# Kernel optimization log

Hardware: AMD Instinct MI355X
Metric: run time of the kernel (lower is better)

Reference implementation:

```python
import jax, jax.numpy as jnp
import numpy as np

B, S, D = 2, 2048, 2048
QC, KVC = 16, 4          # query heads, kv heads (GQA)
HD = D // QC             # head_dim = 128
FF = 8192                # ff_dim = 4 * model_dim
EPS = 1e-5


def rotate_every_two(x):
    x1 = x[..., ::2]
    x2 = x[..., 1::2]
    return jnp.stack((-x2, x1), axis=-1).reshape(*x.shape[:-1], -1)


def apply_rope(x, seq_len, sin, cos):
    sin = sin[:seq_len]
    cos = cos[:seq_len]
    return x * cos + rotate_every_two(x) * sin


def rmsnorm(x, w, eps=EPS):
    xf = x.astype(jnp.float32)
    xf = xf * jax.lax.rsqrt(jnp.square(xf).mean(-1, keepdims=True) + eps)
    return xf.astype(x.dtype) * w


def attention(x, mask, sin, cos, wqkv, wo):
    b, s, d = x.shape
    kv_repeat = QC // KVC
    qkv = x @ wqkv
    q = qkv[..., :D].reshape(b, s, kv_repeat, KVC, HD)
    q = jnp.moveaxis(q, 1, 3)                       # (b, rep, kvc, s, hd)
    q = apply_rope(q, s, sin, cos)
    k, v = jnp.split(qkv[..., D:], 2, axis=-1)
    k = k.reshape(b, s, KVC, HD).swapaxes(1, 2)     # (b, kvc, s, hd)
    v = v.reshape(b, s, KVC, HD).swapaxes(1, 2)
    k = apply_rope(k, s, sin, cos) * (HD ** -0.5)
    k = k[:, None]                                  # (b, 1, kvc, s, hd)
    v = v[:, None]
    a = q @ k.swapaxes(-2, -1)                      # (b, rep, kvc, s, s)
    a = a + mask[:s, :s]
    a = jax.nn.softmax(a, axis=-1)
    o = a @ v                                       # (b, rep, kvc, s, hd)
    o = o.reshape(b, QC, s, HD).swapaxes(1, 2).reshape(b, s, d)
    return o @ wo


def ffn(x, wk, wv):
    k = jnp.square(jax.nn.relu(x @ wk))
    return k @ wv


def setup_inputs() -> dict:
    key = jax.random.key(0)
    ks = jax.random.split(key, 6)
    std = 0.02
    x = jax.random.normal(ks[0], (B, S, D), jnp.float32)
    wqkv = std * jax.random.normal(ks[1], (D, D + 2 * KVC * HD), jnp.float32)
    wo = std * jax.random.normal(ks[2], (D, D), jnp.float32)
    ffn_wk = std * jax.random.normal(ks[3], (D, FF), jnp.float32)
    ffn_wv = std * jax.random.normal(ks[4], (FF, D), jnp.float32)
    norm1_w = jnp.ones((D,), jnp.float32)
    norm2_w = jnp.ones((D,), jnp.float32)
    # GPT-J style interleaved RoPE tables of shape (S, HD)
    pos = jnp.arange(S, dtype=jnp.float32)
    inv_freq = 1.0 / (10000.0 ** (jnp.arange(0, HD, 2, dtype=jnp.float32) / HD))
    freqs = pos[:, None] * inv_freq[None, :]
    rope_sin = jnp.repeat(jnp.sin(freqs), 2, axis=-1)
    rope_cos = jnp.repeat(jnp.cos(freqs), 2, axis=-1)
    # additive causal mask
    mask = jnp.where(jnp.tril(jnp.ones((S, S), bool)), 0.0, -1e9).astype(jnp.float32)
    return dict(x=x, mask=mask, rope_sin=rope_sin, rope_cos=rope_cos,
                wqkv=wqkv, wo=wo, norm1_w=norm1_w, norm2_w=norm2_w,
                ffn_wk=ffn_wk, ffn_wv=ffn_wv)


def reference(x, mask, rope_sin, rope_cos, wqkv, wo, norm1_w, norm2_w, ffn_wk, ffn_wv):
    # pre-norm residual block
    x = x + attention(rmsnorm(x, norm1_w), mask, rope_sin, rope_cos, wqkv, wo)
    x = x + ffn(rmsnorm(x, norm2_w), ffn_wk, ffn_wv)
    return x
```

## Files before the change

### kernel.cpp

```cpp
#include <hip/hip_runtime.h>
#include <hip/hip_bf16.h>
#include <cstdint>
#include <cstddef>
#include <type_traits>

typedef __hip_bfloat16 bf16;
typedef float f32x4 __attribute__((ext_vector_type(4)));
typedef short s16x8 __attribute__((ext_vector_type(8)));

#define BB 2
#define SS 2048
#define DD 2048
#define QCH 16
#define KVH 4
#define HD 128
#define FF 8192

__device__ __forceinline__ float b2f(bf16 v) { return __bfloat162float(v); }
__device__ __forceinline__ bf16 f2b(float v) { return __float2bfloat16(v); }

__device__ __forceinline__ void gl_lds16(const void* g, void* l) {
    __builtin_amdgcn_global_load_lds((const __attribute__((address_space(1))) void*)g,
                                     (__attribute__((address_space(3))) void*)l,
                                     16, 0, 0);
}

#define GBAR __builtin_amdgcn_s_barrier()
#define LGK0 do { asm volatile("s_waitcnt lgkmcnt(0)" ::: "memory"); __builtin_amdgcn_sched_barrier(0); } while (0)
#define VM8  asm volatile("s_waitcnt vmcnt(8)" ::: "memory")

__global__ __launch_bounds__(256) void transpose_cast(const float* __restrict__ src,
                                                      bf16* __restrict__ dst,
                                                      int K, int N) {
    __shared__ float t[32][33];
    int n0 = blockIdx.x * 32, k0 = blockIdx.y * 32;
    int tx = threadIdx.x, ty = threadIdx.y;
#pragma unroll
    for (int j = 0; j < 4; ++j)
        t[ty + j * 8][tx] = src[(size_t)(k0 + ty + j * 8) * N + n0 + tx];
    __syncthreads();
#pragma unroll
    for (int j = 0; j < 4; ++j)
        dst[(size_t)(n0 + ty + j * 8) * K + k0 + tx] = f2b(t[tx][ty + j * 8]);
}

__global__ __launch_bounds__(256) void rmsnorm_k(const float* __restrict__ x,
                                                 const float* __restrict__ w,
                                                 bf16* __restrict__ out) {
    int row = blockIdx.x;
    int tid = threadIdx.x;
    const float* xr = x + (size_t)row * DD + tid * 8;
    f32x4 a0 = *(const f32x4*)xr;
    f32x4 a1 = *(const f32x4*)(xr + 4);
    float f[8];
    float ss = 0.f;
#pragma unroll
    for (int i = 0; i < 4; ++i) { f[i] = a0[i]; f[i + 4] = a1[i]; }
#pragma unroll
    for (int i = 0; i < 8; ++i) ss += f[i] * f[i];
#pragma unroll
    for (int off = 32; off > 0; off >>= 1) ss += __shfl_down(ss, off);
    __shared__ float red[4];
    int lane = tid & 63, wv_ = tid >> 6;
    if (lane == 0) red[wv_] = ss;
    __syncthreads();
    float tot = red[0] + red[1] + red[2] + red[3];
    float scale = rsqrtf(tot * (1.0f / DD) + 1e-5f);
#pragma unroll
    for (int i = 0; i < 8; ++i) {
        int col = tid * 8 + i;
        out[(size_t)row * DD + col] = f2b(f[i] * scale * w[col]);
    }
}

__global__ __launch_bounds__(256) void rmsnorm_add3(const float* __restrict__ pa,
                                                    const float* __restrict__ pb,
                                                    const float* __restrict__ xr,
                                                    const float* __restrict__ w,
                                                    float* __restrict__ x1,
                                                    bf16* __restrict__ out) {
    int row = blockIdx.x;
    int tid = threadIdx.x;
    size_t base = (size_t)row * DD + tid * 8;
    f32x4 a0 = *(const f32x4*)(pa + base);
    f32x4 a1 = *(const f32x4*)(pa + base + 4);
    f32x4 b0 = *(const f32x4*)(pb + base);
    f32x4 b1 = *(const f32x4*)(pb + base + 4);
    f32x4 c0 = *(const f32x4*)(xr + base);
    f32x4 c1 = *(const f32x4*)(xr + base + 4);
    a0 = a0 + b0 + c0;
    a1 = a1 + b1 + c1;
    *(f32x4*)(x1 + base) = a0;
    *(f32x4*)(x1 + base + 4) = a1;
    float f[8];
    float ss = 0.f;
#pragma unroll
    for (int i = 0; i < 4; ++i) { f[i] = a0[i]; f[i + 4] = a1[i]; }
#pragma unroll
    for (int i = 0; i < 8; ++i) ss += f[i] * f[i];
#pragma unroll
    for (int off = 32; off > 0; off >>= 1) ss += __shfl_down(ss, off);
    __shared__ float red[4];
    int lane = tid & 63, wv_ = tid >> 6;
    if (lane == 0) red[wv_] = ss;
    __syncthreads();
    float tot = red[0] + red[1] + red[2] + red[3];
    float scale = rsqrtf(tot * (1.0f / DD) + 1e-5f);
#pragma unroll
    for (int i = 0; i < 8; ++i) {
        int col = tid * 8 + i;
        out[base + i] = f2b(f[i] * scale * w[col]);
    }
}

__global__ __launch_bounds__(256) void add3_k(const float* __restrict__ pa,
                                              const float* __restrict__ pb,
                                              const float* __restrict__ x1,
                                              float* __restrict__ o, int n4) {
    int stride = gridDim.x * 256;
    for (int i = blockIdx.x * 256 + threadIdx.x; i < n4; i += stride) {
        f32x4 a = ((const f32x4*)pa)[i];
        f32x4 b = ((const f32x4*)pb)[i];
        f32x4 c = ((const f32x4*)x1)[i];
        ((f32x4*)o)[i] = a + b + c;
    }
}

__global__ __launch_bounds__(256) void rope_scatter(const bf16* __restrict__ qkv,
                                                    const float* __restrict__ rsin,
                                                    const float* __restrict__ rcos,
                                                    bf16* __restrict__ q_r,
                                                    bf16* __restrict__ k_r,
                                                    bf16* __restrict__ v_t) {
    int p = blockIdx.x * 256 + threadIdx.x;
    int row = p / 1536;
    int c2 = p - row * 1536;
    int col = c2 * 2;
    int b = row >> 11, s = row & 2047;
    size_t qbase = (size_t)row * 3072 + col;
    float e = b2f(qkv[qbase]);
    float o = b2f(qkv[qbase + 1]);
    if (col < 2048) {
        int h = col >> 7, hd = col & 127;
        float cs = rcos[s * HD + hd];
        float sn = rsin[s * HD + hd];
        size_t base = (((size_t)(b * QCH + h)) * SS + s) * HD + hd;
        q_r[base]     = f2b(e * cs - o * sn);
        q_r[base + 1] = f2b(o * cs + e * sn);
    } else if (col < 2560) {
        int cc = col - 2048;
        int kc = cc >> 7, hd = cc & 127;
        float cs = rcos[s * HD + hd];
        float sn = rsin[s * HD + hd];
        const float kscale = 0.08838834764831845f;
        size_t base = (((size_t)(b * KVH + kc)) * SS + s) * HD + hd;
        k_r[base]     = f2b((e * cs - o * sn) * kscale);
        k_r[base + 1] = f2b((o * cs + e * sn) * kscale);
    } else {
        int cc = col - 2560;
        int kc = cc >> 7, hd = cc & 127;
        size_t base = (((size_t)(b * KVH + kc)) * HD + hd) * SS + s;
        v_t[base]      = qkv[qbase];
        v_t[base + SS] = qkv[qbase + 1];
    }
}

template <int EPI, typename CT>
__global__ __launch_bounds__(512) void gemm256(const bf16* __restrict__ A,
                                               const bf16* __restrict__ Bt,
                                               CT* __restrict__ C,
                                               CT* __restrict__ Cp,
                                               int M, int N, int KH, int ldk,
                                               int nsplit) {
    __shared__ __align__(16) bf16 As[2][2][8192];
    __shared__ __align__(16) bf16 Bs[2][2][8192];

    const int tid = threadIdx.x;
    const int w = tid >> 6, lane = tid & 63;
    const int lm = lane & 15, quad = lane >> 4;
    const int wm = w >> 2, wn = w & 3;

    const int cpx = gridDim.x >> 3;
    int sb = (blockIdx.x & 7) * cpx + (blockIdx.x >> 3);
    const int nbx = N >> 8;
    const int ntiles = (M >> 8) * nbx;
    const int kh = (nsplit == 2 && sb >= ntiles) ? 1 : 0;
    sb -= kh * ntiles;
    const int bx = sb % nbx, by = sb / nbx;
    const int m0 = by * 256, n0 = bx * 256;
    CT* Cw = kh ? Cp : C;

    const size_t LD2 = (size_t)ldk * 2;
    const int srow = tid >> 3;
    const int sboff = ((tid & 7) ^ (srow & 7)) * 16;
    const int NT = KH >> 6;

    const char* Abase = (const char*)A + (size_t)m0 * LD2 + (size_t)kh * KH * 2 + sboff;
    const char* Bbase = (const char*)Bt + (size_t)n0 * LD2 + (size_t)kh * KH * 2 + sboff;
    char* lAs = (char*)&As[0][0][0];
    char* lBs = (char*)&Bs[0][0][0];

    auto stA = [&](int db, int h, int t) {
#pragma unroll
        for (int j = 0; j < 2; ++j) {
            int row = h * 128 + j * 64 + srow;
            gl_lds16(Abase + (size_t)row * LD2 + (size_t)t * 128,
                     lAs + (db * 2 + h) * 16384 + j * 8192 + tid * 16);
        }
    };
    auto stB = [&](int db, int h, int t) {
#pragma unroll
        for (int j = 0; j < 2; ++j) {
            int row = h * 128 + j * 64 + srow;
            gl_lds16(Bbase + (size_t)row * LD2 + (size_t)t * 128,
                     lBs + (db * 2 + h) * 16384 + j * 8192 + tid * 16);
        }
    };

    const int c0 = (quad ^ (lm & 7)) * 16;
    const int c1 = ((4 + quad) ^ (lm & 7)) * 16;

    s16x8 a0[4][2], a1[4][2], b0[2][2], b1[2][2];
    f32x4 acc[8][4];
    const f32x4 zero = {0.f, 0.f, 0.f, 0.f};
#pragma unroll
    for (int i = 0; i < 8; ++i)
#pragma unroll
        for (int j = 0; j < 4; ++j) acc[i][j] = zero;

    auto ldA = [&](s16x8 (&a)[4][2], int db, int mh) {
        const char* base = lAs + (db * 2 + wm) * 16384 + (mh * 64 + lm) * 128;
#pragma unroll
        for (int mi = 0; mi < 4; ++mi) {
            a[mi][0] = *(const s16x8*)(base + mi * 2048 + c0);
            a[mi][1] = *(const s16x8*)(base + mi * 2048 + c1);
        }
    };
    auto ldB = [&](s16x8 (&b)[2][2], int db, int nh) {
        const char* base = lBs + (db * 2 + (wn >> 1)) * 16384 + ((wn & 1) * 64 + nh * 32 + lm) * 128;
#pragma unroll
        for (int ni = 0; ni < 2; ++ni) {
            b[ni][0] = *(const s16x8*)(base + ni * 2048 + c0);
            b[ni][1] = *(const s16x8*)(base + ni * 2048 + c1);
        }
    };
    auto mm = [&](s16x8 (&a)[4][2], s16x8 (&b)[2][2], int mh, int nh) {
#pragma unroll
        for (int mi = 0; mi < 4; ++mi)
#pragma unroll
            for (int ni = 0; ni < 2; ++ni)
#pragma unroll
                for (int kk = 0; kk < 2; ++kk)
                    acc[mh * 4 + mi][nh * 2 + ni] = __builtin_amdgcn_mfma_f32_16x16x32_bf16(
                        a[mi][kk], b[ni][kk], acc[mh * 4 + mi][nh * 2 + ni], 0, 0, 0);
    };

    stA(0, 0, 0); stA(0, 1, 0); stB(0, 0, 0); stB(0, 1, 0);
    stA(1, 0, 1); stA(1, 1, 1); stB(1, 0, 1); stB(1, 1, 1);
    VM8;
    GBAR;

    const int NI = NT >> 1;
#pragma unroll 1
    for (int i = 0; i < NI; ++i) {
        int tA = 2 * i + 2; if (tA >= NT) tA = 0;
        int tB = 2 * i + 3; if (tB >= NT) tB = 0;
        ldA(a0, 0, 0); ldB(b0, 0, 0);
        GBAR; LGK0;
        __builtin_amdgcn_s_setprio(1); mm(a0, b0, 0, 0); __builtin_amdgcn_s_setprio(0);
        GBAR;
        ldA(a1, 0, 1); ldB(b1, 0, 1);
        GBAR; LGK0;
        __builtin_amdgcn_s_setprio(1); mm(a1, b1, 1, 1); __builtin_amdgcn_s_setprio(0);
        GBAR;
        stA(0, 0, tA); stA(0, 1, tA);
        GBAR;
        __builtin_amdgcn_s_setprio(1); mm(a0, b1, 0, 1); __builtin_amdgcn_s_setprio(0);
        GBAR;
        stB(0, 0, tA); stB(0, 1, tA);
        GBAR;
        __builtin_amdgcn_s_setprio(1); mm(a1, b0, 1, 0); __builtin_amdgcn_s_setprio(0);
        VM8;
        GBAR;
        ldA(a0, 1, 0); ldB(b0, 1, 0);
        GBAR; LGK0;
        __builtin_amdgcn_s_setprio(1); mm(a0, b0, 0, 0); __builtin_amdgcn_s_setprio(0);
        GBAR;
        ldA(a1, 1, 1); ldB(b1, 1, 1);
        GBAR; LGK0;
        __builtin_amdgcn_s_setprio(1); mm(a1, b1, 1, 1); __builtin_amdgcn_s_setprio(0);
        GBAR;
        stA(1, 0, tB); stA(1, 1, tB);
        GBAR;
        __builtin_amdgcn_s_setprio(1); mm(a0, b1, 0, 1); __builtin_amdgcn_s_setprio(0);
        GBAR;
        stB(1, 0, tB); stB(1, 1, tB);
        GBAR;
        __builtin_amdgcn_s_setprio(1); mm(a1, b0, 1, 0); __builtin_amdgcn_s_setprio(0);
        VM8;
        GBAR;
    }

#pragma unroll
    for (int mi = 0; mi < 8; ++mi)
#pragma unroll
        for (int ni = 0; ni < 4; ++ni) {
            int gr = m0 + wm * 128 + mi * 16 + quad * 4;
            int gc = n0 + wn * 64 + ni * 16 + lm;
#pragma unroll
            for (int r = 0; r < 4; ++r) {
                size_t idx = (size_t)(gr + r) * N + gc;
                float v = acc[mi][ni][r];
                if (EPI == 2) { v = fmaxf(v, 0.f); v = v * v; }
                if constexpr (std::is_same<CT, float>::value) Cw[idx] = v;
                else Cw[idx] = f2b(v);
            }
        }
}

__global__ __launch_bounds__(256) void attn_k(const bf16* __restrict__ q_r,
                                              const bf16* __restrict__ k_r,
                                              const bf16* __restrict__ v_t,
                                              bf16* __restrict__ o_buf) {
    __shared__ __align__(16) bf16 Ks[64 * 128];
    __shared__ __align__(16) bf16 Vs[128 * 64];
    __shared__ __align__(16) bf16 Ps[4][32 * 72];
    const int i = blockIdx.x;
    const int qt = i >> 5, hb = i & 31;
    const int h = hb & 15, b = hb >> 4;
    const int tid = threadIdx.x, w = tid >> 6, lane = tid & 63;
    const int lm = lane & 15, quad = lane >> 4;
    const int kvh = h & (KVH - 1);
    const int qw0 = qt * 128 + w * 32;
    bf16* Pw = &Ps[w][0];

    s16x8 aq[2][4];
#pragma unroll
    for (int mt = 0; mt < 2; ++mt) {
        const bf16* qp = q_r + (((size_t)(b * QCH + h)) * SS + qw0 + mt * 16 + lm) * HD + quad * 8;
#pragma unroll
        for (int c = 0; c < 4; ++c) aq[mt][c] = *(const s16x8*)(qp + c * 32);
    }

    const char* kbase = (const char*)(k_r + ((size_t)(b * KVH + kvh)) * SS * HD);
    const char* vbase = (const char*)(v_t + ((size_t)(b * KVH + kvh)) * HD * SS);

    const int krow = tid >> 4, kslot = tid & 15;
    const int ksrc_off = ((kslot ^ (krow & 15)) * 16);
    const int vrow = tid >> 3, vslot = tid & 7;

    const f32x4 zero = {0.f, 0.f, 0.f, 0.f};
    f32x4 accO[2][8];
#pragma unroll
    for (int mt = 0; mt < 2; ++mt)
#pragma unroll
        for (int ni = 0; ni < 8; ++ni) accO[mt][ni] = zero;
    float lp[2][4] = {{0.f, 0.f, 0.f, 0.f}, {0.f, 0.f, 0.f, 0.f}};

    const int ntiles = 2 * qt + 2;
    for (int kt = 0; kt < ntiles; ++kt) {
        const int kb = kt * 64;
#pragma unroll
        for (int j = 0; j < 4; ++j) {
            int kr = krow + j * 16;
            gl_lds16(kbase + (size_t)(kb + kr) * 256 + ksrc_off, (char*)Ks + tid * 16 + j * 4096);
        }
#pragma unroll
        for (int j = 0; j < 4; ++j) {
            int vr = vrow + j * 32;
            gl_lds16(vbase + (size_t)vr * (SS * 2) + kb * 2 + ((vslot ^ (vr & 7)) * 16),
                     (char*)Vs + tid * 16 + j * 4096);
        }
        __syncthreads();

        const bool active = (kb <= qw0 + 31);
        if (active) {
#pragma unroll
            for (int nt = 0; nt < 4; ++nt) {
                const int krl = nt * 16 + lm;
                s16x8 kf[4];
#pragma unroll
                for (int c = 0; c < 4; ++c)
                    kf[c] = *(const s16x8*)((char*)Ks + krl * 256 + (((c * 4 + quad) ^ lm) * 16));
                const int colk = kb + krl;
#pragma unroll
                for (int mt = 0; mt < 2; ++mt) {
                    f32x4 sc = zero;
#pragma unroll
                    for (int c = 0; c < 4; ++c)
                        sc = __builtin_amdgcn_mfma_f32_16x16x32_bf16(aq[mt][c], kf[c], sc, 0, 0, 0);
#pragma unroll
                    for (int r = 0; r < 4; ++r) {
                        int rowq = qw0 + mt * 16 + quad * 4 + r;
                        float p = (colk <= rowq) ? __expf(sc[r]) : 0.f;
                        lp[mt][r] += p;
                        Pw[(mt * 16 + quad * 4 + r) * 72 + nt * 16 + lm] = f2b(p);
                    }
                }
            }
            s16x8 pf[2][2];
#pragma unroll
            for (int mt = 0; mt < 2; ++mt)
#pragma unroll
                for (int kf2 = 0; kf2 < 2; ++kf2)
                    pf[mt][kf2] = *(const s16x8*)&Pw[(mt * 16 + lm) * 72 + kf2 * 32 + quad * 8];
#pragma unroll
            for (int ni = 0; ni < 8; ++ni) {
                const int vrl = ni * 16 + lm;
#pragma unroll
                for (int kf2 = 0; kf2 < 2; ++kf2) {
                    s16x8 vf = *(const s16x8*)((char*)Vs + vrl * 128 + (((kf2 * 4 + quad) ^ (lm & 7)) * 16));
#pragma unroll
                    for (int mt = 0; mt < 2; ++mt)
                        accO[mt][ni] = __builtin_amdgcn_mfma_f32_16x16x32_bf16(pf[mt][kf2], vf, accO[mt][ni], 0, 0, 0);
                }
            }
        }
        __syncthreads();
    }

#pragma unroll
    for (int mt = 0; mt < 2; ++mt)
#pragma unroll
        for (int r = 0; r < 4; ++r) {
            float l = lp[mt][r];
#pragma unroll
            for (int off = 1; off < 16; off <<= 1) l += __shfl_xor(l, off);
            lp[mt][r] = 1.f / l;
        }

#pragma unroll
    for (int mt = 0; mt < 2; ++mt)
#pragma unroll
        for (int ni = 0; ni < 8; ++ni)
#pragma unroll
            for (int r = 0; r < 4; ++r) {
                int s = qw0 + mt * 16 + quad * 4 + r;
                size_t idx = ((size_t)(b * SS + s)) * DD + h * HD + ni * 16 + lm;
                o_buf[idx] = f2b(accO[mt][ni][r] * lp[mt][r]);
            }
}

extern "C" void kernel_launch(void* const* d_in, const int* in_sizes, int n_in,
                              void* d_out, int out_size, void* d_ws, size_t ws_size,
                              hipStream_t stream) {
    const float* x    = (const float*)d_in[0];
    const float* rsin = (const float*)d_in[2];
    const float* rcos = (const float*)d_in[3];
    const float* wqkv = (const float*)d_in[4];
    const float* wo   = (const float*)d_in[5];
    const float* n1w  = (const float*)d_in[6];
    const float* n2w  = (const float*)d_in[7];
    const float* wk   = (const float*)d_in[8];
    const float* wv   = (const float*)d_in[9];
    float* out = (float*)d_out;

    char* ws = (char*)d_ws;
    size_t off = 0;
    auto allocb = [&](size_t elems) { bf16* p = (bf16*)(ws + off); off += elems * 2; return p; };
    auto allocf = [&](size_t elems) { float* p = (float*)(ws + off); off += elems * 4; return p; };
    bf16* wqkvT = allocb((size_t)3072 * 2048);
    bf16* woT   = allocb((size_t)2048 * 2048);
    bf16* wkT   = allocb((size_t)8192 * 2048);
    bf16* wvT   = allocb((size_t)2048 * 8192);
    bf16* xn    = allocb((size_t)4096 * 2048);
    bf16* qkv   = allocb((size_t)4096 * 3072);
    bf16* q_r   = allocb((size_t)BB * QCH * SS * HD);
    bf16* k_r   = allocb((size_t)BB * KVH * SS * HD);
    bf16* v_t   = allocb((size_t)BB * KVH * HD * SS);
    bf16* ffnh  = allocb((size_t)4096 * 8192);
    float* x1   = allocf((size_t)4096 * 2048);
    float* pwo = (float*)ffnh;
    float* pdn = (float*)qkv;

    dim3 tb(32, 8);
    transpose_cast<<<dim3(3072 / 32, 2048 / 32), tb, 0, stream>>>(wqkv, wqkvT, 2048, 3072);
    transpose_cast<<<dim3(2048 / 32, 2048 / 32), tb, 0, stream>>>(wo, woT, 2048, 2048);
    transpose_cast<<<dim3(8192 / 32, 2048 / 32), tb, 0, stream>>>(wk, wkT, 2048, 8192);
    transpose_cast<<<dim3(2048 / 32, 8192 / 32), tb, 0, stream>>>(wv, wvT, 8192, 2048);

    rmsnorm_k<<<4096, 256, 0, stream>>>(x, n1w, xn);
    gemm256<0, bf16><<<192, 512, 0, stream>>>(xn, wqkvT, qkv, qkv, 4096, 3072, 2048, 2048, 1);
    rope_scatter<<<(4096 * 1536) / 256, 256, 0, stream>>>(qkv, rsin, rcos, q_r, k_r, v_t);
    attn_k<<<512, 256, 0, stream>>>(q_r, k_r, v_t, qkv );
    gemm256<0, float><<<256, 512, 0, stream>>>(qkv, woT, x1, pwo, 4096, 2048, 1024, 2048, 2);
    rmsnorm_add3<<<4096, 256, 0, stream>>>(x1, pwo, x, n2w, x1, xn);
    gemm256<2, bf16><<<512, 512, 0, stream>>>(xn, wkT, ffnh, ffnh, 4096, 8192, 2048, 2048, 1);
    gemm256<0, float><<<256, 512, 0, stream>>>(ffnh, wvT, out, pdn, 4096, 2048, 4096, 8192, 2);
    add3_k<<<2048, 256, 0, stream>>>(out, pdn, x1, out, (4096 * 2048) / 4);
}
```

Before: 811.8 us.

## Restructure GEMM main loop into finer-grained staggered LDS/global prefetch schedule

```diff
diff --git a/kernel.cpp b/kernel.cpp
--- a/kernel.cpp
+++ b/kernel.cpp
@@ -27,7 +27,10 @@
 
 #define GBAR __builtin_amdgcn_s_barrier()
 #define LGK0 do { asm volatile("s_waitcnt lgkmcnt(0)" ::: "memory"); __builtin_amdgcn_sched_barrier(0); } while (0)
-#define VM8  asm volatile("s_waitcnt vmcnt(8)" ::: "memory")
+#define VMC4 asm volatile("s_waitcnt vmcnt(4)" ::: "memory")
+#define VMC0 asm volatile("s_waitcnt vmcnt(0)" ::: "memory")
+#define PRIO1 __builtin_amdgcn_s_setprio(1)
+#define PRIO0 __builtin_amdgcn_s_setprio(0)
 
 __global__ __launch_bounds__(256) void transpose_cast(const float* __restrict__ src,
                                                       bf16* __restrict__ dst,
@@ -166,12 +169,12 @@
 }
 
 template <int EPI, typename CT>
-__global__ __launch_bounds__(512) void gemm256(const bf16* __restrict__ A,
-                                               const bf16* __restrict__ Bt,
-                                               CT* __restrict__ C,
-                                               CT* __restrict__ Cp,
-                                               int M, int N, int KH, int ldk,
-                                               int nsplit) {
+__global__ __launch_bounds__(512, 2) void gemm256(const bf16* __restrict__ A,
+                                                  const bf16* __restrict__ Bt,
+                                                  CT* __restrict__ C,
+                                                  CT* __restrict__ Cp,
+                                                  int M, int N, int KH, int ldk,
+                                                  int nsplit) {
     __shared__ __align__(16) bf16 As[2][2][8192];
     __shared__ __align__(16) bf16 Bs[2][2][8192];
 
@@ -200,21 +203,25 @@
     char* lAs = (char*)&As[0][0][0];
     char* lBs = (char*)&Bs[0][0][0];
 
-    auto stA = [&](int db, int h, int t) {
-#pragma unroll
-        for (int j = 0; j < 2; ++j) {
-            int row = h * 128 + j * 64 + srow;
-            gl_lds16(Abase + (size_t)row * LD2 + (size_t)t * 128,
-                     lAs + (db * 2 + h) * 16384 + j * 8192 + tid * 16);
-        }
+    auto stA = [&](int db, int t) {
+#pragma unroll
+        for (int h = 0; h < 2; ++h)
+#pragma unroll
+            for (int j = 0; j < 2; ++j) {
+                int row = h * 128 + j * 64 + srow;
+                gl_lds16(Abase + (size_t)row * LD2 + (size_t)t * 128,
+                         lAs + (db * 2 + h) * 16384 + j * 8192 + tid * 16);
+            }
     };
-    auto stB = [&](int db, int h, int t) {
-#pragma unroll
-        for (int j = 0; j < 2; ++j) {
-            int row = h * 128 + j * 64 + srow;
-            gl_lds16(Bbase + (size_t)row * LD2 + (size_t)t * 128,
-                     lBs + (db * 2 + h) * 16384 + j * 8192 + tid * 16);
-        }
+    auto stB = [&](int db, int t) {
+#pragma unroll
+        for (int h = 0; h < 2; ++h)
+#pragma unroll
+            for (int j = 0; j < 2; ++j) {
+                int row = h * 128 + j * 64 + srow;
+                gl_lds16(Bbase + (size_t)row * LD2 + (size_t)t * 128,
+                         lBs + (db * 2 + h) * 16384 + j * 8192 + tid * 16);
+            }
     };
 
     const int c0 = (quad ^ (lm & 7)) * 16;
@@ -255,50 +262,37 @@
                         a[mi][kk], b[ni][kk], acc[mh * 4 + mi][nh * 2 + ni], 0, 0, 0);
     };
 
-    stA(0, 0, 0); stA(0, 1, 0); stB(0, 0, 0); stB(0, 1, 0);
-    stA(1, 0, 1); stA(1, 1, 1); stB(1, 0, 1); stB(1, 1, 1);
-    VM8;
+    stA(0, 0); stB(0, 0);
+    VMC0;
     GBAR;
-
-    const int NI = NT >> 1;
+    ldA(a0, 0, 0); ldB(b0, 0, 0);
+    stA(1, 1);
+
 #pragma unroll 1
-    for (int i = 0; i < NI; ++i) {
+    for (int i = 0; i < (NT >> 1); ++i) {
+        const int t1 = 2 * i + 1;
         int tA = 2 * i + 2; if (tA >= NT) tA = 0;
         int tB = 2 * i + 3; if (tB >= NT) tB = 0;
-        ldA(a0, 0, 0); ldB(b0, 0, 0);
-        GBAR; LGK0;
-        __builtin_amdgcn_s_setprio(1); mm(a0, b0, 0, 0); __builtin_amdgcn_s_setprio(0);
-        GBAR;
-        ldA(a1, 0, 1); ldB(b1, 0, 1);
-        GBAR; LGK0;
-        __builtin_amdgcn_s_setprio(1); mm(a1, b1, 1, 1); __builtin_amdgcn_s_setprio(0);
-        GBAR;
-        stA(0, 0, tA); stA(0, 1, tA);
-        GBAR;
-        __builtin_amdgcn_s_setprio(1); mm(a0, b1, 0, 1); __builtin_amdgcn_s_setprio(0);
-        GBAR;
-        stB(0, 0, tA); stB(0, 1, tA);
-        GBAR;
-        __builtin_amdgcn_s_setprio(1); mm(a1, b0, 1, 0); __builtin_amdgcn_s_setprio(0);
-        VM8;
-        GBAR;
-        ldA(a0, 1, 0); ldB(b0, 1, 0);
-        GBAR; LGK0;
-        __builtin_amdgcn_s_setprio(1); mm(a0, b0, 0, 0); __builtin_amdgcn_s_setprio(0);
-        GBAR;
-        ldA(a1, 1, 1); ldB(b1, 1, 1);
-        GBAR; LGK0;
-        __builtin_amdgcn_s_setprio(1); mm(a1, b1, 1, 1); __builtin_amdgcn_s_setprio(0);
-        GBAR;
-        stA(1, 0, tB); stA(1, 1, tB);
-        GBAR;
-        __builtin_amdgcn_s_setprio(1); mm(a0, b1, 0, 1); __builtin_amdgcn_s_setprio(0);
-        GBAR;
-        stB(1, 0, tB); stB(1, 1, tB);
-        GBAR;
-        __builtin_amdgcn_s_setprio(1); mm(a1, b0, 1, 0); __builtin_amdgcn_s_setprio(0);
-        VM8;
-        GBAR;
+        ldB(b1, 0, 1);
+        stB(1, t1);
+        GBAR; LGK0; PRIO1; mm(a0, b0, 0, 0); PRIO0; GBAR;
+        ldA(a1, 0, 1);
+        GBAR; LGK0; PRIO1; mm(a0, b1, 0, 1); PRIO0; VMC4; GBAR;
+        ldA(a0, 1, 0);
+        GBAR; LGK0; PRIO1; mm(a1, b0, 1, 0); PRIO0; VMC0; GBAR;
+        ldB(b0, 1, 0);
+        stA(0, tA);
+        GBAR; LGK0; PRIO1; mm(a1, b1, 1, 1); PRIO0; GBAR;
+        ldB(b1, 1, 1);
+        stB(0, tA);
+        GBAR; LGK0; PRIO1; mm(a0, b0, 0, 0); PRIO0; GBAR;
+        ldA(a1, 1, 1);
+        GBAR; LGK0; PRIO1; mm(a0, b1, 0, 1); PRIO0; VMC4; GBAR;
+        ldA(a0, 0, 0);
+        GBAR; LGK0; PRIO1; mm(a1, b0, 1, 0); PRIO0; VMC0; GBAR;
+        ldB(b0, 0, 0);
+        stA(1, tB);
+        GBAR; LGK0; PRIO1; mm(a1, b1, 1, 1); PRIO0; GBAR;
     }
 
 #pragma unroll
```

New measurement: 830.7 us. 1.02x slower.
